# Kernel tuning notes

Hardware: AMD Instinct MI355X
Metric: run time of the kernel (lower is better)

## Reference

```python
import jax, jax.numpy as jnp
import numpy as np

DIM, QK, GS, DEPTH, VOCAB, ROT = 16, 128, 256, 8, 1024, 32
EPS = 1e-5


def scale_norm(x, g):
    # ScaleNorm: x / max(||x|| * dim^-0.5, eps) * g
    norm = jnp.linalg.norm(x, axis=-1, keepdims=True) * (DIM ** -0.5)
    return x / jnp.clip(norm, EPS) * g


def rotate_half(x):
    # interleaved pairs: (x0,x1,x2,x3,...) -> (-x1,x0,-x3,x2,...)
    xr = x.reshape(x.shape[:-1] + (-1, 2))
    a, b = xr[..., 0], xr[..., 1]
    return jnp.stack((-b, a), axis=-1).reshape(x.shape)


def apply_rotary(x, cos, sin):
    # rotary applied to first ROT dims only
    xr, xp = x[..., :ROT], x[..., ROT:]
    return jnp.concatenate([xr * cos + rotate_half(xr) * sin, xp], axis=-1)


def flash_layer(x, p, cos, sin, keymask, n):
    b = x.shape[0]
    normed = scale_norm(x, p['norm_g'])
    # shift_tokens: first half of channels shifted forward by one position
    xs, xp = jnp.split(normed, 2, axis=-1)
    xs = jnp.pad(xs, ((0, 0), (1, 0), (0, 0)))[:, :-1]
    normed = jnp.concatenate([xs, xp], axis=-1)
    hid = jax.nn.silu(normed @ p['Wh'] + p['bh'])  # [b,n,64]
    v, gate = jnp.split(hid, 2, axis=-1)           # each [b,n,32]
    qk = jax.nn.silu(normed @ p['Wqk'] + p['bqk'])  # [b,n,128]
    offs = qk[..., None, :] * p['gamma'] + p['beta']  # [b,n,4,128]
    quad_q, lin_q, quad_k, lin_k = [apply_rotary(offs[..., i, :], cos, sin) for i in range(4)]
    pad = (-n) % GS
    grp = lambda t: jnp.pad(t, ((0, 0), (0, pad), (0, 0))).reshape(b, -1, GS, t.shape[-1])
    quad_q, quad_k, lin_q, lin_k, vg = map(grp, (quad_q, quad_k, lin_q, lin_k, v))
    # quadratic (local, within-group) attention with ReLU^2
    sim = jnp.einsum('bgid,bgjd->bgij', quad_q, quad_k) / GS
    attn = jnp.square(jax.nn.relu(sim)) * keymask  # mask out padded keys
    quad_out = jnp.einsum('bgij,bgjd->bgid', attn, vg)
    # linear (global, across-group) attention, reduced over groups
    lin_kv = jnp.einsum('bgnd,bgne->bde', lin_k, vg) / n
    lin_out = jnp.einsum('bgnd,bde->bgne', lin_q, lin_kv)
    out = (quad_out + lin_out).reshape(b, -1, v.shape[-1])[:, :n]
    out = gate * out
    return out @ p['Wo'] + p['bo'] + x


def forward(kmer_data, token_emb, pos_scale, norm_g, Wh, bh, Wqk, bqk, gamma, beta, Wo, bo, final_g, Wl, bl, W1, b1, W2, b2):
    b, n = kmer_data.shape
    x = token_emb[kmer_data]  # [b,n,16]
    t = jnp.arange(n, dtype=jnp.float32)
    # ScaledSinuEmbedding
    inv = 1.0 / (10000.0 ** (jnp.arange(0, DIM, 2, dtype=jnp.float32) / DIM))
    sinu = t[:, None] * inv[None, :]
    pos = jnp.concatenate([jnp.sin(sinu), jnp.cos(sinu)], axis=-1) * pos_scale
    x = x + pos
    # rotary tables (dim 32, interleaved repeat)
    rinv = 1.0 / (10000.0 ** (jnp.arange(0, ROT, 2, dtype=jnp.float32) / ROT))
    rf = jnp.repeat(t[:, None] * rinv[None, :], 2, axis=-1)  # [n,32]
    cos, sin = jnp.cos(rf), jnp.sin(rf)
    # key mask for padded positions (996 -> 1024)
    pad = (-n) % GS
    keymask = jnp.pad(jnp.ones((n,), jnp.float32), (0, pad)).reshape(1, -1, 1, GS)
    for i in range(DEPTH):
        p = dict(norm_g=norm_g[i], Wh=Wh[i], bh=bh[i], Wqk=Wqk[i], bqk=bqk[i],
                 gamma=gamma[i], beta=beta[i], Wo=Wo[i], bo=bo[i])
        x = flash_layer(x, p, cos, sin, keymask, n)
    logits = scale_norm(x, final_g) @ Wl + bl  # [b,n,1024]
    h = jnp.max(logits, axis=-1)               # AdaptiveMaxPool1d(1) + Flatten -> [b,n]
    h = jax.nn.relu(h @ W1 + b1)
    return h @ W2 + b2                          # [b,1]


def setup_inputs() -> dict:
    key = jax.random.key(0)
    ks = jax.random.split(key, 12)
    r = lambda k, shape, s: jax.random.normal(k, shape, jnp.float32) * s
    return {
        'kmer_data': jax.random.randint(ks[0], (128, 996), 0, VOCAB),
        'token_emb': r(ks[1], (VOCAB, DIM), 1.0),
        'pos_scale': jnp.float32(1.0),
        'norm_g': jnp.ones((DEPTH,), jnp.float32),
        'Wh': r(ks[2], (DEPTH, DIM, 64), 0.1),
        'bh': jnp.zeros((DEPTH, 64), jnp.float32),
        'Wqk': r(ks[3], (DEPTH, DIM, QK), 0.1),
        'bqk': jnp.zeros((DEPTH, QK), jnp.float32),
        'gamma': 1.0 + r(ks[4], (DEPTH, 4, QK), 0.02),
        'beta': r(ks[5], (DEPTH, 4, QK), 0.02),
        'Wo': r(ks[6], (DEPTH, 32, DIM), 0.1),
        'bo': jnp.zeros((DEPTH, DIM), jnp.float32),
        'final_g': jnp.float32(1.0),
        'Wl': r(ks[7], (DIM, VOCAB), 0.1),
        'bl': jnp.zeros((VOCAB,), jnp.float32),
        'W1': r(ks[8], (996, 32), 0.05),
        'b1': jnp.zeros((32,), jnp.float32),
        'W2': r(ks[9], (32, 1), 0.1),
        'b2': jnp.zeros((1,), jnp.float32),
    }


def reference(kmer_data, token_emb, pos_scale, norm_g, Wh, bh, Wqk, bqk, gamma, beta, Wo, bo, final_g, Wl, bl, W1, b1, W2, b2):
    return forward(kmer_data, token_emb, pos_scale, norm_g, Wh, bh, Wqk, bqk,
                   gamma, beta, Wo, bo, final_g, Wl, bl, W1, b1, W2, b2)
```

## Files before the change

### kernel.cpp

```cpp
#include <hip/hip_runtime.h>

typedef short s16x8 __attribute__((ext_vector_type(8)));
typedef float f32x4 __attribute__((ext_vector_type(4)));

#define NB    128
#define NTOK  996
#define NPAD  1024
#define NGRP  4
#define GSZ   256
#define NLAY  8

__device__ __forceinline__ float bf2f(unsigned short u){
    unsigned int v = ((unsigned int)u) << 16;
    return __uint_as_float(v);
}
__device__ __forceinline__ unsigned short f2bf(float f){
    unsigned int x = __float_as_uint(f);
    unsigned int r = (x + 0x7fffu + ((x >> 16) & 1u)) >> 16;
    return (unsigned short)r;
}
__device__ __forceinline__ unsigned int packbf(float a, float b){
    return (unsigned int)f2bf(a) | ((unsigned int)f2bf(b) << 16);
}
__device__ __forceinline__ float silu(float v){
    return v / (1.0f + __expf(-v));
}

__device__ __forceinline__ s16x8 derive_core(const unsigned short* __restrict__ qrow, int d0,
        float4 g0, float4 g1, float4 b0, float4 b1,
        const float* __restrict__ rp, bool rot){
    uint4 u = *(const uint4*)(qrow + d0);
    float y0 = bf2f((unsigned short)(u.x & 0xffffu))*g0.x + b0.x;
    float y1 = bf2f((unsigned short)(u.x >> 16))    *g0.y + b0.y;
    float y2 = bf2f((unsigned short)(u.y & 0xffffu))*g0.z + b0.z;
    float y3 = bf2f((unsigned short)(u.y >> 16))    *g0.w + b0.w;
    float y4 = bf2f((unsigned short)(u.z & 0xffffu))*g1.x + b1.x;
    float y5 = bf2f((unsigned short)(u.z >> 16))    *g1.y + b1.y;
    float y6 = bf2f((unsigned short)(u.w & 0xffffu))*g1.z + b1.z;
    float y7 = bf2f((unsigned short)(u.w >> 16))    *g1.w + b1.w;
    if (rot){
        float4 c4 = *(const float4*)(rp);
        float4 s4 = *(const float4*)(rp + 16);
        float a;
        a = y0; y0 = a*c4.x - y1*s4.x; y1 = y1*c4.x + a*s4.x;
        a = y2; y2 = a*c4.y - y3*s4.y; y3 = y3*c4.y + a*s4.y;
        a = y4; y4 = a*c4.z - y5*s4.z; y5 = y5*c4.z + a*s4.z;
        a = y6; y6 = a*c4.w - y7*s4.w; y7 = y7*c4.w + a*s4.w;
    }
    union { unsigned int uu[4]; s16x8 s; } r;
    r.uu[0] = packbf(y0, y1);
    r.uu[1] = packbf(y2, y3);
    r.uu[2] = packbf(y4, y5);
    r.uu[3] = packbf(y6, y7);
    return r.s;
}

__global__ __launch_bounds__(256) void k_embed(const int* __restrict__ kmer,
                                               const float* __restrict__ emb,
                                               const float* __restrict__ ps,
                                               float* __restrict__ x,
                                               float* __restrict__ rope){
    int gid = blockIdx.x * 256 + threadIdx.x;
    if (gid < NPAD){
        float tf2 = (float)gid;
        #pragma unroll
        for (int i = 0; i < 16; i++){
            float inv = expf(((float)(2*i) / 32.0f) * -9.210340371976184f);
            float ang = tf2 * inv;
            rope[gid*32 + i]      = cosf(ang);
            rope[gid*32 + 16 + i] = sinf(ang);
        }
    }
    if (gid >= NB * NTOK) return;
    int b = gid / NTOK;
    int tt = gid - b * NTOK;
    int idx = kmer[gid];
    const float* er = emb + (size_t)idx * 16;
    float pscale = ps[0];
    float tf = (float)tt;
    float* xr = x + (size_t)gid * 16;
    #pragma unroll
    for (int i = 0; i < 8; i++){
        float inv = expf(((float)(2*i) / 16.0f) * -9.210340371976184f);
        float ang = tf * inv;
        xr[i]     = er[i]     + sinf(ang) * pscale;
        xr[8 + i] = er[8 + i] + cosf(ang) * pscale;
    }
}

__global__ __launch_bounds__(256, 2) void k_pre(const float* __restrict__ x,
                                             const float* __restrict__ Wh, const float* __restrict__ bh,
                                             const float* __restrict__ Wqk, const float* __restrict__ bqk,
                                             const float* __restrict__ norm_g,
                                             const float* __restrict__ gamma, const float* __restrict__ beta,
                                             const float* __restrict__ rope, int layer,
                                             unsigned short* __restrict__ qk,
                                             unsigned short* __restrict__ vT,
                                             unsigned short* __restrict__ gateb,
                                             float* __restrict__ linkvp){
    __shared__ __align__(16) unsigned short WcT[192 * 40];
    __shared__ unsigned int nrm[256][4];
    __shared__ __align__(16) unsigned char arena[23040];
    unsigned short* As = (unsigned short*)arena;
    unsigned short* LkT = (unsigned short*)arena;
    unsigned short* Vt  = (unsigned short*)(arena + 18432);
    int tid = threadIdx.x;
    int qt = blockIdx.x & 3, b = blockIdx.x >> 2;
    const float* Whl = Wh  + (size_t)layer * 1024;
    const float* Wql = Wqk + (size_t)layer * 2048;
    const float* gLin = gamma + (size_t)layer * 512 + 384;
    const float* bLin = beta  + (size_t)layer * 512 + 384;
    for (int i = tid; i < 1024; i += 256){ int d = i >> 6, c = i & 63;  WcT[c*40 + d] = f2bf(Whl[i]); }
    for (int i = tid; i < 2048; i += 256){ int d = i >> 7, c = i & 127; WcT[(64 + c)*40 + d] = f2bf(Wql[i]); }
    if (tid < 192){
        int i = tid;
        float bv = (i < 64) ? bh[layer*64 + i] : bqk[layer*128 + (i - 64)];
        WcT[i*40 + 16] = f2bf(bv);
        WcT[i*40 + 17] = 0;
        unsigned int* zz = (unsigned int*)(WcT + i*40 + 18);
        #pragma unroll
        for (int k = 0; k < 7; k++) zz[k] = 0u;
    }
    int tt = qt*256 + tid;
    int tsafe = tt < NTOK ? tt : (NTOK - 1);
    float g = norm_g[layer];
    unsigned int* dd = (unsigned int*)(As + tid * 40);
    {
        const float4* xr4 = (const float4*)(x + ((size_t)b*NTOK + tsafe) * 16);
        float cur[16];
        float s2 = 0.f;
        #pragma unroll
        for (int c = 0; c < 4; c++){
            float4 v4 = xr4[c];
            cur[4*c] = v4.x; cur[4*c+1] = v4.y; cur[4*c+2] = v4.z; cur[4*c+3] = v4.w;
        }
        #pragma unroll
        for (int d = 0; d < 16; d++) s2 += cur[d]*cur[d];
        float sc = g / fmaxf(sqrtf(s2) * 0.25f, 1e-5f);
        #pragma unroll
        for (int i = 0; i < 4; i++) nrm[tid][i] = packbf(cur[2*i]*sc, cur[2*i+1]*sc);
        #pragma unroll
        for (int i = 0; i < 4; i++) dd[4 + i] = packbf(cur[8 + 2*i]*sc, cur[9 + 2*i]*sc);
        dd[8] = 0x00003f80u;
        #pragma unroll
        for (int i = 9; i < 16; i++) dd[i] = 0u;
    }
    __syncthreads();
    if (tt == 0){
        #pragma unroll
        for (int i = 0; i < 4; i++) dd[i] = 0u;
    } else if (tid > 0){
        #pragma unroll
        for (int i = 0; i < 4; i++) dd[i] = nrm[tid - 1][i];
    } else {
        const float4* xp4 = (const float4*)(x + ((size_t)b*NTOK + tt - 1) * 16);
        float prv[16]; float p2 = 0.f;
        #pragma unroll
        for (int c = 0; c < 4; c++){
            float4 v4 = xp4[c];
            prv[4*c] = v4.x; prv[4*c+1] = v4.y; prv[4*c+2] = v4.z; prv[4*c+3] = v4.w;
        }
        #pragma unroll
        for (int d = 0; d < 16; d++) p2 += prv[d]*prv[d];
        float sp = g / fmaxf(sqrtf(p2) * 0.25f, 1e-5f);
        #pragma unroll
        for (int i = 0; i < 4; i++) dd[i] = packbf(prv[2*i]*sp, prv[2*i+1]*sp);
    }
    __syncthreads();
    int w = tid >> 6, lane = tid & 63, m16 = lane & 15, quad = lane >> 4;
    s16x8 wf[12];
    #pragma unroll
    for (int mi = 0; mi < 12; mi++)
        wf[mi] = *(const s16x8*)(WcT + (mi*16 + m16)*40 + quad*8);
    s16x8 bfr[4];
    #pragma unroll
    for (int nt = 0; nt < 4; nt++)
        bfr[nt] = *(const s16x8*)(As + ((w*64 + nt*16 + m16))*40 + quad*8);
    __syncthreads();
    f32x4 zacc = {0.f,0.f,0.f,0.f};
    f32x4 lacc[2][2] = {{{0,0,0,0},{0,0,0,0}},{{0,0,0,0},{0,0,0,0}}};
    #pragma unroll
    for (int nt = 0; nt < 4; nt++){
        int tloc = w*64 + nt*16 + m16;
        int ttk = qt*256 + tloc;
        bool tv = ttk < NTOK;
        int c = w*16 + m16;
        size_t rowq = ((size_t)b*NPAD + ttk);
        #pragma unroll
        for (int mi = 0; mi < 12; mi++){
            f32x4 r = __builtin_amdgcn_mfma_f32_16x16x32_bf16(wf[mi], bfr[nt], zacc, 0, 0, 0);
            float sv[4];
            #pragma unroll
            for (int reg = 0; reg < 4; reg++) sv[reg] = silu(r[reg]);
            int wc0 = mi*16 + quad*4;
            if (mi < 2){
                #pragma unroll
                for (int reg = 0; reg < 4; reg++){
                    unsigned short pv = tv ? f2bf(sv[reg]) : (unsigned short)0;
                    vT[((size_t)b*32 + wc0 + reg)*NPAD + ttk] = pv;
                    Vt[(wc0 + reg)*72 + c] = pv;
                }
            } else if (mi < 4){
                *(uint2*)(gateb + rowq*32 + (wc0 - 32)) = make_uint2(packbf(sv[0],sv[1]), packbf(sv[2],sv[3]));
            } else {
                int qd = wc0 - 64;
                *(uint2*)(qk + rowq*128 + qd) = make_uint2(packbf(sv[0],sv[1]), packbf(sv[2],sv[3]));
                float y0 = sv[0]*gLin[qd]   + bLin[qd];
                float y1 = sv[1]*gLin[qd+1] + bLin[qd+1];
                float y2 = sv[2]*gLin[qd+2] + bLin[qd+2];
                float y3 = sv[3]*gLin[qd+3] + bLin[qd+3];
                if (qd < 32){
                    const float* rp = rope + ttk*32 + (qd >> 1);
                    float c0 = rp[0], s0 = rp[16], c1 = rp[1], s1 = rp[17];
                    float a;
                    a = y0; y0 = a*c0 - y1*s0; y1 = y1*c0 + a*s0;
                    a = y2; y2 = a*c1 - y3*s1; y3 = y3*c1 + a*s1;
                }
                LkT[(qd+0)*72 + c] = f2bf(y0);
                LkT[(qd+1)*72 + c] = f2bf(y1);
                LkT[(qd+2)*72 + c] = f2bf(y2);
                LkT[(qd+3)*72 + c] = f2bf(y3);
            }
        }
        __syncthreads();
        #pragma unroll
        for (int ks2 = 0; ks2 < 2; ks2++){
            s16x8 a0 = *(const s16x8*)(LkT + ((2*w  )*16 + m16)*72 + ks2*32 + quad*8);
            s16x8 a1 = *(const s16x8*)(LkT + ((2*w+1)*16 + m16)*72 + ks2*32 + quad*8);
            s16x8 b0 = *(const s16x8*)(Vt + (m16)*72 + ks2*32 + quad*8);
            s16x8 b1 = *(const s16x8*)(Vt + (16 + m16)*72 + ks2*32 + quad*8);
            lacc[0][0] = __builtin_amdgcn_mfma_f32_16x16x32_bf16(a0, b0, lacc[0][0], 0,0,0);
            lacc[0][1] = __builtin_amdgcn_mfma_f32_16x16x32_bf16(a0, b1, lacc[0][1], 0,0,0);
            lacc[1][0] = __builtin_amdgcn_mfma_f32_16x16x32_bf16(a1, b0, lacc[1][0], 0,0,0);
            lacc[1][1] = __builtin_amdgcn_mfma_f32_16x16x32_bf16(a1, b1, lacc[1][1], 0,0,0);
        }
        __syncthreads();
    }
    const float invn = 1.0f / 996.0f;
    #pragma unroll
    for (int i = 0; i < 2; i++){
        #pragma unroll
        for (int j = 0; j < 2; j++){
            int e = j*16 + m16;
            #pragma unroll
            for (int reg = 0; reg < 4; reg++){
                int d = (2*w + i)*16 + quad*4 + reg;
                linkvp[(((size_t)qt*NB + b)*32 + e)*128 + d] = lacc[i][j][reg] * invn;
            }
        }
    }
}

#define KD_BYTES (64*136*2)
#define PW_BYTES (8*32*72*2)
__global__ __launch_bounds__(512, 2) void k_quad(const unsigned short* __restrict__ qk,
                                              const unsigned short* __restrict__ vT,
                                              const unsigned short* __restrict__ gateb,
                                              const float* __restrict__ linkvp,
                                              const float* __restrict__ rope,
                                              const float* __restrict__ gamma, const float* __restrict__ beta,
                                              int layer,
                                              const float* __restrict__ Wo, const float* __restrict__ bo,
                                              float* __restrict__ x){
    __shared__ __align__(16) unsigned char smem[KD_BYTES + PW_BYTES];
    __shared__ __align__(16) unsigned short LkBs[32 * 136];
    __shared__ float sWo[512];
    __shared__ float sbo[16];
    unsigned short* Kd = (unsigned short*)smem;
    unsigned short* Pw = (unsigned short*)(smem + KD_BYTES);
    int tid = threadIdx.x;
    int blk = blockIdx.x;
    int g = blk & 3, b = blk >> 2;
    int tg0 = g * GSZ;
    const float* gamL = gamma + (size_t)layer * 512;
    const float* betL = beta  + (size_t)layer * 512;
    sWo[tid] = Wo[layer*512 + tid];
    if (tid < 16) sbo[tid] = bo[layer*16 + tid];

    int w = tid >> 6, lane = tid & 63, m16 = lane & 15, quad = lane >> 4;

    int tqA = tg0 + w*32 + m16;
    int tqB = tqA + 16;
    const unsigned short* qrowA = qk + ((size_t)b*NPAD + tqA)*128;
    const unsigned short* qrowB = qk + ((size_t)b*NPAD + tqB)*128;
    const float* rpA = rope + tqA*32 + quad*4;
    const float* rpB = rope + tqB*32 + quad*4;
    s16x8 qf[2][4];
    #pragma unroll
    for (int ks = 0; ks < 4; ks++){
        int d0 = ks*32 + quad*8;
        float4 g0 = *(const float4*)(gamL + d0), g1 = *(const float4*)(gamL + d0 + 4);
        float4 b0 = *(const float4*)(betL + d0), b1 = *(const float4*)(betL + d0 + 4);
        bool rot = (ks == 0) && (quad < 4);
        qf[0][ks] = derive_core(qrowA, d0, g0,g1,b0,b1, rpA, rot);
        qf[1][ks] = derive_core(qrowB, d0, g0,g1,b0,b1, rpB, rot);
    }

    const float* gK = gamL + 256;
    const float* bK = betL + 256;
    f32x4 oacc[2][2] = {{{0,0,0,0},{0,0,0,0}},{{0,0,0,0},{0,0,0,0}}};
    unsigned short* myP = Pw + w*32*72;

    for (int ch = 0; ch < 4; ch++){
        __syncthreads();
        {
            int r = tid >> 3, seg = (tid & 7) * 16;
            int tk = tg0 + ch*64 + r;
            const unsigned short* krow = qk + ((size_t)b*NPAD + tk)*128 + seg;
            unsigned int* dst = (unsigned int*)(Kd + r*136 + seg);
            #pragma unroll
            for (int h = 0; h < 2; h++){
                uint4 u = ((const uint4*)krow)[h];
                unsigned int uu[4] = {u.x, u.y, u.z, u.w};
                float y[8];
                #pragma unroll
                for (int k = 0; k < 4; k++){
                    int d = h*8 + 2*k;
                    y[2*k]   = bf2f((unsigned short)(uu[k] & 0xffffu)) * gK[seg + d]     + bK[seg + d];
                    y[2*k+1] = bf2f((unsigned short)(uu[k] >> 16))     * gK[seg + d + 1] + bK[seg + d + 1];
                }
                if (seg < 32){
                    const float* rp = rope + tk*32 + (seg >> 1) + h*4;
                    #pragma unroll
                    for (int p = 0; p < 4; p++){
                        float c = rp[p], s = rp[16 + p];
                        float a = y[2*p], d = y[2*p+1];
                        y[2*p]   = a*c - d*s;
                        y[2*p+1] = d*c + a*s;
                    }
                }
                #pragma unroll
                for (int k = 0; k < 4; k++) dst[h*4 + k] = packbf(y[2*k], y[2*k+1]);
            }
        }
        __syncthreads();
        #pragma unroll
        for (int np = 0; np < 2; np++){
            f32x4 s00 = {0,0,0,0}, s01 = {0,0,0,0}, s10 = {0,0,0,0}, s11 = {0,0,0,0};
            #pragma unroll
            for (int ks = 0; ks < 4; ks++){
                s16x8 kf0 = *(const s16x8*)(Kd + ((np*2  )*16 + m16)*136 + ks*32 + quad*8);
                s16x8 kf1 = *(const s16x8*)(Kd + ((np*2+1)*16 + m16)*136 + ks*32 + quad*8);
                s00 = __builtin_amdgcn_mfma_f32_16x16x32_bf16(qf[0][ks], kf0, s00, 0,0,0);
                s01 = __builtin_amdgcn_mfma_f32_16x16x32_bf16(qf[0][ks], kf1, s01, 0,0,0);
                s10 = __builtin_amdgcn_mfma_f32_16x16x32_bf16(qf[1][ks], kf0, s10, 0,0,0);
                s11 = __builtin_amdgcn_mfma_f32_16x16x32_bf16(qf[1][ks], kf1, s11, 0,0,0);
            }
            #pragma unroll
            for (int j = 0; j < 2; j++){
                int kl = (np*2 + j)*16 + m16;
                bool kv = (tg0 + ch*64 + kl) < NTOK;
                #pragma unroll
                for (int reg = 0; reg < 4; reg++){
                    float a0 = fmaxf(j ? s01[reg] : s00[reg], 0.0f);
                    float a1 = fmaxf(j ? s11[reg] : s10[reg], 0.0f);
                    a0 = a0 * a0;
                    a1 = a1 * a1;
                    myP[(quad*4 + reg)*72 + kl]      = kv ? f2bf(a0) : (unsigned short)0;
                    myP[(16 + quad*4 + reg)*72 + kl] = kv ? f2bf(a1) : (unsigned short)0;
                }
            }
        }
        #pragma unroll
        for (int i = 0; i < 2; i++){
            #pragma unroll
            for (int ks = 0; ks < 2; ks++){
                s16x8 pa = *(const s16x8*)(myP + (i*16 + m16)*72 + ks*32 + quad*8);
                s16x8 vf0 = *(const s16x8*)(vT + ((size_t)b*32 + m16)*NPAD + tg0 + ch*64 + ks*32 + quad*8);
                s16x8 vf1 = *(const s16x8*)(vT + ((size_t)b*32 + 16 + m16)*NPAD + tg0 + ch*64 + ks*32 + quad*8);
                oacc[i][0] = __builtin_amdgcn_mfma_f32_16x16x32_bf16(pa, vf0, oacc[i][0], 0,0,0);
                oacc[i][1] = __builtin_amdgcn_mfma_f32_16x16x32_bf16(pa, vf1, oacc[i][1], 0,0,0);
            }
        }
    }
    const float qsc = 1.0f / 65536.0f;
    #pragma unroll
    for (int i = 0; i < 2; i++)
        #pragma unroll
        for (int j = 0; j < 2; j++)
            oacc[i][j] = oacc[i][j] * qsc;
    {
        int e = tid >> 4, dbase = (tid & 15) * 8;
        float s[8];
        #pragma unroll
        for (int k = 0; k < 8; k++) s[k] = 0.f;
        #pragma unroll
        for (int part = 0; part < 4; part++){
            const float* src = linkvp + (((size_t)part*NB + b)*32 + e)*128 + dbase;
            float4 u0 = *(const float4*)src;
            float4 u1 = *(const float4*)(src + 4);
            s[0]+=u0.x; s[1]+=u0.y; s[2]+=u0.z; s[3]+=u0.w;
            s[4]+=u1.x; s[5]+=u1.y; s[6]+=u1.z; s[7]+=u1.w;
        }
        unsigned int* dst = (unsigned int*)(LkBs + e*136 + dbase);
        #pragma unroll
        for (int k = 0; k < 4; k++) dst[k] = packbf(s[2*k], s[2*k+1]);
    }
    __syncthreads();
    {
        const float* gamQ = gamL + 128;
        const float* betQ = betL + 128;
        #pragma unroll
        for (int ks = 0; ks < 4; ks++){
            int d0 = ks*32 + quad*8;
            float4 g0 = *(const float4*)(gamQ + d0), g1 = *(const float4*)(gamQ + d0 + 4);
            float4 b0 = *(const float4*)(betQ + d0), b1 = *(const float4*)(betQ + d0 + 4);
            bool rot = (ks == 0) && (quad < 4);
            s16x8 lf0 = derive_core(qrowA, d0, g0,g1,b0,b1, rpA, rot);
            s16x8 lf1 = derive_core(qrowB, d0, g0,g1,b0,b1, rpB, rot);
            #pragma unroll
            for (int j = 0; j < 2; j++){
                s16x8 lb = *(const s16x8*)(LkBs + (j*16 + m16)*136 + ks*32 + quad*8);
                oacc[0][j] = __builtin_amdgcn_mfma_f32_16x16x32_bf16(lf0, lb, oacc[0][j], 0,0,0);
                oacc[1][j] = __builtin_amdgcn_mfma_f32_16x16x32_bf16(lf1, lb, oacc[1][j], 0,0,0);
            }
        }
    }
    float* Obw = (float*)smem + w*1056;
    #pragma unroll
    for (int i = 0; i < 2; i++)
        #pragma unroll
        for (int j = 0; j < 2; j++)
            #pragma unroll
            for (int reg = 0; reg < 4; reg++)
                Obw[(i*16 + quad*4 + reg)*33 + j*16 + m16] = oacc[i][j][reg];
    {
        int r = lane >> 1, dp = (lane & 1) * 8;
        int p = tg0 + w*32 + r;
        if (p < NTOK){
            const unsigned short* gr = gateb + ((size_t)b*NPAD + p)*32;
            float* xr = x + ((size_t)b * NTOK + p)*16 + dp;
            float4 x0 = *(const float4*)xr;
            float4 x1 = *(const float4*)(xr + 4);
            float a[8] = { sbo[dp]+x0.x, sbo[dp+1]+x0.y, sbo[dp+2]+x0.z, sbo[dp+3]+x0.w,
                           sbo[dp+4]+x1.x, sbo[dp+5]+x1.y, sbo[dp+6]+x1.z, sbo[dp+7]+x1.w };
            #pragma unroll
            for (int eh = 0; eh < 4; eh++){
                uint4 gu = *(const uint4*)(gr + eh*8);
                unsigned int gg[4] = {gu.x, gu.y, gu.z, gu.w};
                #pragma unroll
                for (int k = 0; k < 4; k++){
                    float gv0 = bf2f((unsigned short)(gg[k] & 0xffffu));
                    float gv1 = bf2f((unsigned short)(gg[k] >> 16));
                    int e = eh*8 + 2*k;
                    float ov0 = Obw[r*33 + e] * gv0;
                    float ov1 = Obw[r*33 + e + 1] * gv1;
                    const float* wr0 = &sWo[e*16 + dp];
                    const float* wr1 = &sWo[(e+1)*16 + dp];
                    #pragma unroll
                    for (int kk = 0; kk < 8; kk++) a[kk] += ov0 * wr0[kk] + ov1 * wr1[kk];
                }
            }
            *(float4*)xr = make_float4(a[0],a[1],a[2],a[3]);
            *(float4*)(xr+4) = make_float4(a[4],a[5],a[6],a[7]);
        }
    }
}

__global__ __launch_bounds__(256) void k_head(const float* __restrict__ x,
                                              const float* __restrict__ Wl, const float* __restrict__ bl,
                                              const float* __restrict__ fg, float* __restrict__ h){
    __shared__ __align__(16) unsigned short WlT[512 * 40];
    __shared__ __align__(16) unsigned short As[256 * 40];
    int tid = threadIdx.x;
    int gid0 = blockIdx.x * 256;
    {
        int t = gid0 + tid;
        const float4* xr4 = (const float4*)(x + (size_t)t * 16);
        float cur[16]; float s2 = 0.f;
        #pragma unroll
        for (int c = 0; c < 4; c++){
            float4 v4 = xr4[c];
            cur[4*c] = v4.x; cur[4*c+1] = v4.y; cur[4*c+2] = v4.z; cur[4*c+3] = v4.w;
        }
        #pragma unroll
        for (int d = 0; d < 16; d++) s2 += cur[d]*cur[d];
        float sc = fg[0] / fmaxf(sqrtf(s2) * 0.25f, 1e-5f);
        unsigned int* dd = (unsigned int*)(As + tid * 40);
        #pragma unroll
        for (int i = 0; i < 8; i++) dd[i] = packbf(cur[2*i]*sc, cur[2*i+1]*sc);
        dd[8] = 0x00003f80u;
        #pragma unroll
        for (int i = 9; i < 16; i++) dd[i] = 0u;
    }
    int w = tid >> 6, lane = tid & 63, m16 = lane & 15, quad = lane >> 4;
    f32x4 vm[4];
    #pragma unroll
    for (int i = 0; i < 4; i++) vm[i] = (f32x4){-3e38f,-3e38f,-3e38f,-3e38f};
    for (int half = 0; half < 2; half++){
        __syncthreads();
        for (int i = tid; i < 8192; i += 256){
            int d = i >> 9, c = i & 511;
            WlT[c*40 + d] = f2bf(Wl[(size_t)d*1024 + half*512 + c]);
        }
        for (int i = tid; i < 512; i += 256){
            WlT[i*40 + 16] = f2bf(bl[half*512 + i]);
            WlT[i*40 + 17] = 0;
            unsigned int* zz = (unsigned int*)(WlT + i*40 + 18);
            #pragma unroll
            for (int k = 0; k < 7; k++) zz[k] = 0u;
        }
        __syncthreads();
        s16x8 af[4];
        #pragma unroll
        for (int i = 0; i < 4; i++)
            af[i] = *(const s16x8*)(As + (w*64 + i*16 + m16)*40 + quad*8);
        f32x4 zacc = {0,0,0,0};
        for (int nt = 0; nt < 32; nt++){
            s16x8 bf = *(const s16x8*)(WlT + (nt*16 + m16)*40 + quad*8);
            #pragma unroll
            for (int i = 0; i < 4; i++){
                f32x4 r = __builtin_amdgcn_mfma_f32_16x16x32_bf16(af[i], bf, zacc, 0,0,0);
                #pragma unroll
                for (int reg = 0; reg < 4; reg++)
                    vm[i][reg] = fmaxf(vm[i][reg], r[reg]);
            }
        }
    }
    #pragma unroll
    for (int i = 0; i < 4; i++){
        #pragma unroll
        for (int off = 1; off < 16; off <<= 1){
            #pragma unroll
            for (int reg = 0; reg < 4; reg++)
                vm[i][reg] = fmaxf(vm[i][reg], __shfl_xor(vm[i][reg], off, 64));
        }
    }
    if (m16 == 0){
        #pragma unroll
        for (int i = 0; i < 4; i++){
            int t0 = gid0 + w*64 + i*16 + quad*4;
            #pragma unroll
            for (int reg = 0; reg < 4; reg++)
                h[t0 + reg] = vm[i][reg];
        }
    }
}

__global__ __launch_bounds__(256) void k_final(const float* __restrict__ h,
                                               const float* __restrict__ W1, const float* __restrict__ b1,
                                               const float* __restrict__ W2, const float* __restrict__ b2,
                                               float* __restrict__ out){
    int b = blockIdx.x;
    int tid = threadIdx.x;
    int j = tid & 31, part = tid >> 5;
    float acc = 0.f;
    for (int i = part; i < NTOK; i += 8)
        acc += h[(size_t)b*NTOK + i] * W1[(size_t)i*32 + j];
    __shared__ float red[8][33];
    red[part][j] = acc;
    __syncthreads();
    if (tid < 32){
        float s = b1[tid];
        #pragma unroll
        for (int p = 0; p < 8; p++) s += red[p][tid];
        s = fmaxf(s, 0.f);
        red[0][tid] = s * W2[tid];
    }
    __syncthreads();
    if (tid == 0){
        float s = b2[0];
        #pragma unroll
        for (int jj = 0; jj < 32; jj++) s += red[0][jj];
        out[b] = s;
    }
}

extern "C" void kernel_launch(void* const* d_in, const int* in_sizes, int n_in,
                              void* d_out, int out_size, void* d_ws, size_t ws_size,
                              hipStream_t stream){
    const int*   kmer  = (const int*)d_in[0];
    const float* emb   = (const float*)d_in[1];
    const float* ps    = (const float*)d_in[2];
    const float* ng    = (const float*)d_in[3];
    const float* Wh    = (const float*)d_in[4];
    const float* bh    = (const float*)d_in[5];
    const float* Wqk   = (const float*)d_in[6];
    const float* bqk   = (const float*)d_in[7];
    const float* gamma = (const float*)d_in[8];
    const float* beta  = (const float*)d_in[9];
    const float* Wo    = (const float*)d_in[10];
    const float* bo    = (const float*)d_in[11];
    const float* fg    = (const float*)d_in[12];
    const float* Wl    = (const float*)d_in[13];
    const float* bl    = (const float*)d_in[14];
    const float* W1    = (const float*)d_in[15];
    const float* b1    = (const float*)d_in[16];
    const float* W2    = (const float*)d_in[17];
    const float* b2    = (const float*)d_in[18];
    float* out = (float*)d_out;

    char* wsp = (char*)d_ws;
    float* x = (float*)wsp;                     wsp += (size_t)NB*NTOK*16*4;
    unsigned short* qk = (unsigned short*)wsp;  wsp += (size_t)NB*NPAD*128*2;
    unsigned short* vT = (unsigned short*)wsp;  wsp += (size_t)NB*32*NPAD*2;
    unsigned short* gateb = (unsigned short*)wsp; wsp += (size_t)NB*NPAD*32*2;
    float* linkvp = (float*)wsp;                wsp += (size_t)4*NB*32*128*4;
    float* rope = (float*)wsp;                  wsp += (size_t)NPAD*32*4;
    float* h = (float*)wsp;                     wsp += (size_t)NB*NTOK*4;

    k_embed<<<(NB*NTOK + 255)/256, 256, 0, stream>>>(kmer, emb, ps, x, rope);
    for (int layer = 0; layer < NLAY; layer++){
        k_pre<<<NB*4, 256, 0, stream>>>(x, Wh, bh, Wqk, bqk, ng, gamma, beta, rope, layer, qk, vT, gateb, linkvp);
        k_quad<<<NB*NGRP, 512, 0, stream>>>(qk, vT, gateb, linkvp, rope, gamma, beta, layer, Wo, bo, x);
    }
    k_head<<<NB*NTOK/256, 256, 0, stream>>>(x, Wl, bl, fg, h);
    k_final<<<NB, 256, 0, stream>>>(h, W1, b1, W2, b2, out);
}
```

Baseline: 833.4 us.

## Widen k_pre to 512 threads, stage outputs via LDS, prefetch K and V in k_quad

k_pre now runs 512 threads per block, with each wave handling 32 tokens instead of 64. Its weight fragments are reloaded from LDS per MFMA rather than held in registers. qk, gate, vT and linkvp writes are buffered and emitted as coalesced vector stores through LDS transposes, and the shifted-token neighbour write goes straight into LDS, which drops one barrier. k_quad register-prefetches the next K chunk and its rope values, loads the V fragments early, hoists the gate and residual loads ahead of the epilogue, and raises launch bounds to 4 waves per SIMD occupancy. Together these aim to hide global latency and improve store coalescing, at the cost of more register and LDS pressure.

```diff
diff --git a/kernel.cpp b/kernel.cpp
--- a/kernel.cpp
+++ b/kernel.cpp
@@ -88,7 +88,7 @@
     }
 }
 
-__global__ __launch_bounds__(256, 2) void k_pre(const float* __restrict__ x,
+__global__ __launch_bounds__(512, 4) void k_pre(const float* __restrict__ x,
                                              const float* __restrict__ Wh, const float* __restrict__ bh,
                                              const float* __restrict__ Wqk, const float* __restrict__ bqk,
                                              const float* __restrict__ norm_g,
@@ -98,20 +98,19 @@
                                              unsigned short* __restrict__ vT,
                                              unsigned short* __restrict__ gateb,
                                              float* __restrict__ linkvp){
-    __shared__ __align__(16) unsigned short WcT[192 * 40];
-    __shared__ unsigned int nrm[256][4];
-    __shared__ __align__(16) unsigned char arena[23040];
-    unsigned short* As = (unsigned short*)arena;
-    unsigned short* LkT = (unsigned short*)arena;
-    unsigned short* Vt  = (unsigned short*)(arena + 18432);
+    __shared__ __align__(16) unsigned char sm[58880];
+    unsigned short* WcT = (unsigned short*)sm;
+    unsigned short* As  = (unsigned short*)(sm + 15360);
+    unsigned short* LkT = (unsigned short*)(sm + 15360);
+    unsigned short* Vt  = (unsigned short*)(sm + 50176);
     int tid = threadIdx.x;
     int qt = blockIdx.x & 3, b = blockIdx.x >> 2;
     const float* Whl = Wh  + (size_t)layer * 1024;
     const float* Wql = Wqk + (size_t)layer * 2048;
     const float* gLin = gamma + (size_t)layer * 512 + 384;
     const float* bLin = beta  + (size_t)layer * 512 + 384;
-    for (int i = tid; i < 1024; i += 256){ int d = i >> 6, c = i & 63;  WcT[c*40 + d] = f2bf(Whl[i]); }
-    for (int i = tid; i < 2048; i += 256){ int d = i >> 7, c = i & 127; WcT[(64 + c)*40 + d] = f2bf(Wql[i]); }
+    for (int i = tid; i < 1024; i += 512){ int d = i >> 6, c2 = i & 63;  WcT[c2*40 + d] = f2bf(Whl[i]); }
+    for (int i = tid; i < 2048; i += 512){ int d = i >> 7, c2 = i & 127; WcT[(64 + c2)*40 + d] = f2bf(Wql[i]); }
     if (tid < 192){
         int i = tid;
         float bv = (i < 64) ? bh[layer*64 + i] : bqk[layer*128 + (i - 64)];
@@ -121,90 +120,94 @@
         #pragma unroll
         for (int k = 0; k < 7; k++) zz[k] = 0u;
     }
-    int tt = qt*256 + tid;
-    int tsafe = tt < NTOK ? tt : (NTOK - 1);
     float g = norm_g[layer];
-    unsigned int* dd = (unsigned int*)(As + tid * 40);
-    {
+    if (tid < 256){
+        int tt = qt*256 + tid;
+        int tsafe = tt < NTOK ? tt : (NTOK - 1);
+        unsigned int* dd = (unsigned int*)(As + tid * 40);
         const float4* xr4 = (const float4*)(x + ((size_t)b*NTOK + tsafe) * 16);
         float cur[16];
         float s2 = 0.f;
         #pragma unroll
-        for (int c = 0; c < 4; c++){
-            float4 v4 = xr4[c];
-            cur[4*c] = v4.x; cur[4*c+1] = v4.y; cur[4*c+2] = v4.z; cur[4*c+3] = v4.w;
+        for (int c2 = 0; c2 < 4; c2++){
+            float4 v4 = xr4[c2];
+            cur[4*c2] = v4.x; cur[4*c2+1] = v4.y; cur[4*c2+2] = v4.z; cur[4*c2+3] = v4.w;
         }
         #pragma unroll
         for (int d = 0; d < 16; d++) s2 += cur[d]*cur[d];
         float sc = g / fmaxf(sqrtf(s2) * 0.25f, 1e-5f);
         #pragma unroll
-        for (int i = 0; i < 4; i++) nrm[tid][i] = packbf(cur[2*i]*sc, cur[2*i+1]*sc);
-        #pragma unroll
         for (int i = 0; i < 4; i++) dd[4 + i] = packbf(cur[8 + 2*i]*sc, cur[9 + 2*i]*sc);
         dd[8] = 0x00003f80u;
         #pragma unroll
         for (int i = 9; i < 16; i++) dd[i] = 0u;
-    }
-    __syncthreads();
-    if (tt == 0){
-        #pragma unroll
-        for (int i = 0; i < 4; i++) dd[i] = 0u;
-    } else if (tid > 0){
-        #pragma unroll
-        for (int i = 0; i < 4; i++) dd[i] = nrm[tid - 1][i];
-    } else {
-        const float4* xp4 = (const float4*)(x + ((size_t)b*NTOK + tt - 1) * 16);
-        float prv[16]; float p2 = 0.f;
-        #pragma unroll
-        for (int c = 0; c < 4; c++){
-            float4 v4 = xp4[c];
-            prv[4*c] = v4.x; prv[4*c+1] = v4.y; prv[4*c+2] = v4.z; prv[4*c+3] = v4.w;
-        }
-        #pragma unroll
-        for (int d = 0; d < 16; d++) p2 += prv[d]*prv[d];
-        float sp = g / fmaxf(sqrtf(p2) * 0.25f, 1e-5f);
-        #pragma unroll
-        for (int i = 0; i < 4; i++) dd[i] = packbf(prv[2*i]*sp, prv[2*i+1]*sp);
+        if (tid < 255){
+            unsigned int* ddn = (unsigned int*)(As + (tid+1) * 40);
+            #pragma unroll
+            for (int i = 0; i < 4; i++) ddn[i] = packbf(cur[2*i]*sc, cur[2*i+1]*sc);
+        }
+        if (tid == 0){
+            if (tt == 0){
+                dd[0] = 0u; dd[1] = 0u; dd[2] = 0u; dd[3] = 0u;
+            } else {
+                const float4* xp4 = (const float4*)(x + ((size_t)b*NTOK + tt - 1) * 16);
+                float prv[16]; float p2 = 0.f;
+                #pragma unroll
+                for (int c2 = 0; c2 < 4; c2++){
+                    float4 v4 = xp4[c2];
+                    prv[4*c2] = v4.x; prv[4*c2+1] = v4.y; prv[4*c2+2] = v4.z; prv[4*c2+3] = v4.w;
+                }
+                #pragma unroll
+                for (int d = 0; d < 16; d++) p2 += prv[d]*prv[d];
+                float sp = g / fmaxf(sqrtf(p2) * 0.25f, 1e-5f);
+                #pragma unroll
+                for (int i = 0; i < 4; i++) dd[i] = packbf(prv[2*i]*sp, prv[2*i+1]*sp);
+            }
+        }
     }
     __syncthreads();
     int w = tid >> 6, lane = tid & 63, m16 = lane & 15, quad = lane >> 4;
-    s16x8 wf[12];
-    #pragma unroll
-    for (int mi = 0; mi < 12; mi++)
-        wf[mi] = *(const s16x8*)(WcT + (mi*16 + m16)*40 + quad*8);
-    s16x8 bfr[4];
-    #pragma unroll
-    for (int nt = 0; nt < 4; nt++)
-        bfr[nt] = *(const s16x8*)(As + ((w*64 + nt*16 + m16))*40 + quad*8);
+    s16x8 bfr[2];
+    #pragma unroll
+    for (int nt = 0; nt < 2; nt++)
+        bfr[nt] = *(const s16x8*)(As + (w*32 + nt*16 + m16)*40 + quad*8);
     __syncthreads();
     f32x4 zacc = {0.f,0.f,0.f,0.f};
-    f32x4 lacc[2][2] = {{{0,0,0,0},{0,0,0,0}},{{0,0,0,0},{0,0,0,0}}};
-    #pragma unroll
-    for (int nt = 0; nt < 4; nt++){
-        int tloc = w*64 + nt*16 + m16;
-        int ttk = qt*256 + tloc;
+    f32x4 lacc[2] = {{0,0,0,0},{0,0,0,0}};
+    unsigned int qku[2][8][2];
+    unsigned int gu_[2][2][2];
+    unsigned int vpk[2][2][2];
+    int c = w*16 + m16;
+    #pragma unroll
+    for (int nt = 0; nt < 2; nt++){
+        int ttk = qt*256 + w*32 + nt*16 + m16;
         bool tv = ttk < NTOK;
-        int c = w*16 + m16;
-        size_t rowq = ((size_t)b*NPAD + ttk);
         #pragma unroll
         for (int mi = 0; mi < 12; mi++){
-            f32x4 r = __builtin_amdgcn_mfma_f32_16x16x32_bf16(wf[mi], bfr[nt], zacc, 0, 0, 0);
+            s16x8 wfm = *(const s16x8*)(WcT + (mi*16 + m16)*40 + quad*8);
+            f32x4 r = __builtin_amdgcn_mfma_f32_16x16x32_bf16(wfm, bfr[nt], zacc, 0, 0, 0);
             float sv[4];
             #pragma unroll
             for (int reg = 0; reg < 4; reg++) sv[reg] = silu(r[reg]);
             int wc0 = mi*16 + quad*4;
             if (mi < 2){
-                #pragma unroll
-                for (int reg = 0; reg < 4; reg++){
-                    unsigned short pv = tv ? f2bf(sv[reg]) : (unsigned short)0;
-                    vT[((size_t)b*32 + wc0 + reg)*NPAD + ttk] = pv;
-                    Vt[(wc0 + reg)*72 + c] = pv;
-                }
+                unsigned short p0 = tv ? f2bf(sv[0]) : (unsigned short)0;
+                unsigned short p1 = tv ? f2bf(sv[1]) : (unsigned short)0;
+                unsigned short p2 = tv ? f2bf(sv[2]) : (unsigned short)0;
+                unsigned short p3 = tv ? f2bf(sv[3]) : (unsigned short)0;
+                Vt[(wc0+0)*136 + c] = p0;
+                Vt[(wc0+1)*136 + c] = p1;
+                Vt[(wc0+2)*136 + c] = p2;
+                Vt[(wc0+3)*136 + c] = p3;
+                vpk[nt][mi][0] = (unsigned int)p0 | ((unsigned int)p1 << 16);
+                vpk[nt][mi][1] = (unsigned int)p2 | ((unsigned int)p3 << 16);
             } else if (mi < 4){
-                *(uint2*)(gateb + rowq*32 + (wc0 - 32)) = make_uint2(packbf(sv[0],sv[1]), packbf(sv[2],sv[3]));
+                gu_[nt][mi-2][0] = packbf(sv[0], sv[1]);
+                gu_[nt][mi-2][1] = packbf(sv[2], sv[3]);
             } else {
                 int qd = wc0 - 64;
-                *(uint2*)(qk + rowq*128 + qd) = make_uint2(packbf(sv[0],sv[1]), packbf(sv[2],sv[3]));
+                qku[nt][mi-4][0] = packbf(sv[0], sv[1]);
+                qku[nt][mi-4][1] = packbf(sv[2], sv[3]);
                 float y0 = sv[0]*gLin[qd]   + bLin[qd];
                 float y1 = sv[1]*gLin[qd+1] + bLin[qd+1];
                 float y2 = sv[2]*gLin[qd+2] + bLin[qd+2];
@@ -216,44 +219,74 @@
                     a = y0; y0 = a*c0 - y1*s0; y1 = y1*c0 + a*s0;
                     a = y2; y2 = a*c1 - y3*s1; y3 = y3*c1 + a*s1;
                 }
-                LkT[(qd+0)*72 + c] = f2bf(y0);
-                LkT[(qd+1)*72 + c] = f2bf(y1);
-                LkT[(qd+2)*72 + c] = f2bf(y2);
-                LkT[(qd+3)*72 + c] = f2bf(y3);
+                LkT[(qd+0)*136 + c] = f2bf(y0);
+                LkT[(qd+1)*136 + c] = f2bf(y1);
+                LkT[(qd+2)*136 + c] = f2bf(y2);
+                LkT[(qd+3)*136 + c] = f2bf(y3);
             }
         }
         __syncthreads();
         #pragma unroll
-        for (int ks2 = 0; ks2 < 2; ks2++){
-            s16x8 a0 = *(const s16x8*)(LkT + ((2*w  )*16 + m16)*72 + ks2*32 + quad*8);
-            s16x8 a1 = *(const s16x8*)(LkT + ((2*w+1)*16 + m16)*72 + ks2*32 + quad*8);
-            s16x8 b0 = *(const s16x8*)(Vt + (m16)*72 + ks2*32 + quad*8);
-            s16x8 b1 = *(const s16x8*)(Vt + (16 + m16)*72 + ks2*32 + quad*8);
-            lacc[0][0] = __builtin_amdgcn_mfma_f32_16x16x32_bf16(a0, b0, lacc[0][0], 0,0,0);
-            lacc[0][1] = __builtin_amdgcn_mfma_f32_16x16x32_bf16(a0, b1, lacc[0][1], 0,0,0);
-            lacc[1][0] = __builtin_amdgcn_mfma_f32_16x16x32_bf16(a1, b0, lacc[1][0], 0,0,0);
-            lacc[1][1] = __builtin_amdgcn_mfma_f32_16x16x32_bf16(a1, b1, lacc[1][1], 0,0,0);
+        for (int ks2 = 0; ks2 < 4; ks2++){
+            s16x8 a  = *(const s16x8*)(LkT + (w*16 + m16)*136 + ks2*32 + quad*8);
+            s16x8 b0 = *(const s16x8*)(Vt + (m16)*136 + ks2*32 + quad*8);
+            s16x8 b1 = *(const s16x8*)(Vt + (16 + m16)*136 + ks2*32 + quad*8);
+            lacc[0] = __builtin_amdgcn_mfma_f32_16x16x32_bf16(a, b0, lacc[0], 0,0,0);
+            lacc[1] = __builtin_amdgcn_mfma_f32_16x16x32_bf16(a, b1, lacc[1], 0,0,0);
         }
         __syncthreads();
     }
-    const float invn = 1.0f / 996.0f;
-    #pragma unroll
-    for (int i = 0; i < 2; i++){
-        #pragma unroll
-        for (int j = 0; j < 2; j++){
-            int e = j*16 + m16;
-            #pragma unroll
-            for (int reg = 0; reg < 4; reg++){
-                int d = (2*w + i)*16 + quad*4 + reg;
-                linkvp[(((size_t)qt*NB + b)*32 + e)*128 + d] = lacc[i][j][reg] * invn;
-            }
+    #pragma unroll
+    for (int nt = 0; nt < 2; nt++){
+        size_t rowq = (size_t)b*NPAD + qt*256 + w*32 + nt*16 + m16;
+        #pragma unroll
+        for (int mi8 = 0; mi8 < 8; mi8++)
+            *(uint2*)(qk + rowq*128 + mi8*16 + quad*4) = make_uint2(qku[nt][mi8][0], qku[nt][mi8][1]);
+        *(uint2*)(gateb + rowq*32 + quad*4)      = make_uint2(gu_[nt][0][0], gu_[nt][0][1]);
+        *(uint2*)(gateb + rowq*32 + 16 + quad*4) = make_uint2(gu_[nt][1][0], gu_[nt][1][1]);
+    }
+    {
+        unsigned short* mv = (unsigned short*)sm + w*1280;
+        #pragma unroll
+        for (int nt = 0; nt < 2; nt++){
+            #pragma unroll
+            for (int mi = 0; mi < 2; mi++){
+                int e0 = mi*16 + quad*4;
+                mv[(e0+0)*40 + nt*16 + m16] = (unsigned short)(vpk[nt][mi][0] & 0xffffu);
+                mv[(e0+1)*40 + nt*16 + m16] = (unsigned short)(vpk[nt][mi][0] >> 16);
+                mv[(e0+2)*40 + nt*16 + m16] = (unsigned short)(vpk[nt][mi][1] & 0xffffu);
+                mv[(e0+3)*40 + nt*16 + m16] = (unsigned short)(vpk[nt][mi][1] >> 16);
+            }
+        }
+        #pragma unroll
+        for (int r2 = 0; r2 < 2; r2++){
+            int e = r2*16 + (lane >> 2);
+            int cc = (lane & 3) * 8;
+            s16x8 vv = *(const s16x8*)(mv + e*40 + cc);
+            *(s16x8*)(vT + ((size_t)b*32 + e)*NPAD + qt*256 + w*32 + cc) = vv;
+        }
+    }
+    {
+        float* ml = (float*)(sm + 20480) + w*512;
+        const float invn = 1.0f / 996.0f;
+        #pragma unroll
+        for (int j = 0; j < 2; j++)
+            #pragma unroll
+            for (int reg = 0; reg < 4; reg++)
+                ml[(j*16 + m16)*16 + quad*4 + reg] = lacc[j][reg] * invn;
+        #pragma unroll
+        for (int r2 = 0; r2 < 2; r2++){
+            int e = r2*16 + (lane >> 2);
+            int dc = (lane & 3) * 4;
+            float4 vv = *(const float4*)(ml + e*16 + dc);
+            *(float4*)(linkvp + (((size_t)qt*NB + b)*32 + e)*128 + w*16 + dc) = vv;
         }
     }
 }
 
 #define KD_BYTES (64*136*2)
 #define PW_BYTES (8*32*72*2)
-__global__ __launch_bounds__(512, 2) void k_quad(const unsigned short* __restrict__ qk,
+__global__ __launch_bounds__(512, 4) void k_quad(const unsigned short* __restrict__ qk,
                                               const unsigned short* __restrict__ vT,
                                               const unsigned short* __restrict__ gateb,
                                               const float* __restrict__ linkvp,
@@ -301,16 +334,34 @@
     f32x4 oacc[2][2] = {{{0,0,0,0},{0,0,0,0}},{{0,0,0,0},{0,0,0,0}}};
     unsigned short* myP = Pw + w*32*72;
 
+    int kr = tid >> 3, seg = (tid & 7) * 16;
+    uint4 pku0, pku1;
+    float4 prc0, prc1, prs0, prs1;
+    auto LOADK = [&](int ch){
+        int tk = tg0 + ch*64 + kr;
+        const unsigned short* krow = qk + ((size_t)b*NPAD + tk)*128 + seg;
+        pku0 = ((const uint4*)krow)[0];
+        pku1 = ((const uint4*)krow)[1];
+        const float* rpk = rope + (seg < 32 ? (tk*32 + (seg >> 1)) : 0);
+        prc0 = *(const float4*)(rpk);
+        prs0 = *(const float4*)(rpk + 16);
+        prc1 = *(const float4*)(rpk + 4);
+        prs1 = *(const float4*)(rpk + 20);
+    };
+    LOADK(0);
+
     for (int ch = 0; ch < 4; ch++){
-        __syncthreads();
+        s16x8 vf[2][2];
+        #pragma unroll
+        for (int ks2 = 0; ks2 < 2; ks2++){
+            vf[ks2][0] = *(const s16x8*)(vT + ((size_t)b*32 + m16)*NPAD + tg0 + ch*64 + ks2*32 + quad*8);
+            vf[ks2][1] = *(const s16x8*)(vT + ((size_t)b*32 + 16 + m16)*NPAD + tg0 + ch*64 + ks2*32 + quad*8);
+        }
+        uint4 kd0, kd1;
         {
-            int r = tid >> 3, seg = (tid & 7) * 16;
-            int tk = tg0 + ch*64 + r;
-            const unsigned short* krow = qk + ((size_t)b*NPAD + tk)*128 + seg;
-            unsigned int* dst = (unsigned int*)(Kd + r*136 + seg);
             #pragma unroll
             for (int h = 0; h < 2; h++){
-                uint4 u = ((const uint4*)krow)[h];
+                uint4 u = h ? pku1 : pku0;
                 unsigned int uu[4] = {u.x, u.y, u.z, u.w};
                 float y[8];
                 #pragma unroll
@@ -320,19 +371,27 @@
                     y[2*k+1] = bf2f((unsigned short)(uu[k] >> 16))     * gK[seg + d + 1] + bK[seg + d + 1];
                 }
                 if (seg < 32){
-                    const float* rp = rope + tk*32 + (seg >> 1) + h*4;
+                    float cc[4], ss[4];
+                    if (h){ cc[0]=prc1.x; cc[1]=prc1.y; cc[2]=prc1.z; cc[3]=prc1.w;
+                            ss[0]=prs1.x; ss[1]=prs1.y; ss[2]=prs1.z; ss[3]=prs1.w; }
+                    else  { cc[0]=prc0.x; cc[1]=prc0.y; cc[2]=prc0.z; cc[3]=prc0.w;
+                            ss[0]=prs0.x; ss[1]=prs0.y; ss[2]=prs0.z; ss[3]=prs0.w; }
                     #pragma unroll
-                    for (int p = 0; p < 4; p++){
-                        float c = rp[p], s = rp[16 + p];
-                        float a = y[2*p], d = y[2*p+1];
-                        y[2*p]   = a*c - d*s;
-                        y[2*p+1] = d*c + a*s;
+                    for (int p2 = 0; p2 < 4; p2++){
+                        float a = y[2*p2], d2 = y[2*p2+1];
+                        y[2*p2]   = a*cc[p2] - d2*ss[p2];
+                        y[2*p2+1] = d2*cc[p2] + a*ss[p2];
                     }
                 }
-                #pragma unroll
-                for (int k = 0; k < 4; k++) dst[h*4 + k] = packbf(y[2*k], y[2*k+1]);
-            }
-        }
+                uint4 kk = make_uint4(packbf(y[0],y[1]), packbf(y[2],y[3]),
+                                      packbf(y[4],y[5]), packbf(y[6],y[7]));
+                if (h) kd1 = kk; else kd0 = kk;
+            }
+        }
+        __syncthreads();
+        *(uint4*)(Kd + kr*136 + seg)     = kd0;
+        *(uint4*)(Kd + kr*136 + seg + 8) = kd1;
+        if (ch < 3) LOADK(ch + 1);
         __syncthreads();
         #pragma unroll
         for (int np = 0; np < 2; np++){
@@ -364,12 +423,10 @@
         #pragma unroll
         for (int i = 0; i < 2; i++){
             #pragma unroll
-            for (int ks = 0; ks < 2; ks++){
-                s16x8 pa = *(const s16x8*)(myP + (i*16 + m16)*72 + ks*32 + quad*8);
-                s16x8 vf0 = *(const s16x8*)(vT + ((size_t)b*32 + m16)*NPAD + tg0 + ch*64 + ks*32 + quad*8);
-                s16x8 vf1 = *(const s16x8*)(vT + ((size_t)b*32 + 16 + m16)*NPAD + tg0 + ch*64 + ks*32 + quad*8);
-                oacc[i][0] = __builtin_amdgcn_mfma_f32_16x16x32_bf16(pa, vf0, oacc[i][0], 0,0,0);
-                oacc[i][1] = __builtin_amdgcn_mfma_f32_16x16x32_bf16(pa, vf1, oacc[i][1], 0,0,0);
+            for (int ks2 = 0; ks2 < 2; ks2++){
+                s16x8 pa = *(const s16x8*)(myP + (i*16 + m16)*72 + ks2*32 + quad*8);
+                oacc[i][0] = __builtin_amdgcn_mfma_f32_16x16x32_bf16(pa, vf[ks2][0], oacc[i][0], 0,0,0);
+                oacc[i][1] = __builtin_amdgcn_mfma_f32_16x16x32_bf16(pa, vf[ks2][1], oacc[i][1], 0,0,0);
             }
         }
     }
@@ -397,6 +454,17 @@
         for (int k = 0; k < 4; k++) dst[k] = packbf(s[2*k], s[2*k+1]);
     }
     __syncthreads();
+    int pr = lane >> 1, dp2 = (lane & 1) * 8;
+    int p = tg0 + w*32 + pr;
+    bool pvld = p < NTOK;
+    int psafe = pvld ? p : (NTOK - 1);
+    const unsigned short* gr = gateb + ((size_t)b*NPAD + psafe)*32;
+    uint4 egu[4];
+    #pragma unroll
+    for (int eh = 0; eh < 4; eh++) egu[eh] = *(const uint4*)(gr + eh*8);
+    float* xr = x + ((size_t)b*NTOK + psafe)*16 + dp2;
+    float4 ex0 = *(const float4*)xr;
+    float4 ex1 = *(const float4*)(xr + 4);
     {
         const float* gamQ = gamL + 128;
         const float* betQ = betL + 128;
@@ -424,36 +492,27 @@
             #pragma unroll
             for (int reg = 0; reg < 4; reg++)
                 Obw[(i*16 + quad*4 + reg)*33 + j*16 + m16] = oacc[i][j][reg];
-    {
-        int r = lane >> 1, dp = (lane & 1) * 8;
-        int p = tg0 + w*32 + r;
-        if (p < NTOK){
-            const unsigned short* gr = gateb + ((size_t)b*NPAD + p)*32;
-            float* xr = x + ((size_t)b * NTOK + p)*16 + dp;
-            float4 x0 = *(const float4*)xr;
-            float4 x1 = *(const float4*)(xr + 4);
-            float a[8] = { sbo[dp]+x0.x, sbo[dp+1]+x0.y, sbo[dp+2]+x0.z, sbo[dp+3]+x0.w,
-                           sbo[dp+4]+x1.x, sbo[dp+5]+x1.y, sbo[dp+6]+x1.z, sbo[dp+7]+x1.w };
-            #pragma unroll
-            for (int eh = 0; eh < 4; eh++){
-                uint4 gu = *(const uint4*)(gr + eh*8);
-                unsigned int gg[4] = {gu.x, gu.y, gu.z, gu.w};
+    if (pvld){
+        float a[8] = { sbo[dp2]+ex0.x, sbo[dp2+1]+ex0.y, sbo[dp2+2]+ex0.z, sbo[dp2+3]+ex0.w,
+                       sbo[dp2+4]+ex1.x, sbo[dp2+5]+ex1.y, sbo[dp2+6]+ex1.z, sbo[dp2+7]+ex1.w };
+        #pragma unroll
+        for (int eh = 0; eh < 4; eh++){
+            unsigned int gg[4] = {egu[eh].x, egu[eh].y, egu[eh].z, egu[eh].w};
+            #pragma unroll
+            for (int k = 0; k < 4; k++){
+                float gv0 = bf2f((unsigned short)(gg[k] & 0xffffu));
+                float gv1 = bf2f((unsigned short)(gg[k] >> 16));
+                int e = eh*8 + 2*k;
+                float ov0 = Obw[pr*33 + e] * gv0;
+                float ov1 = Obw[pr*33 + e + 1] * gv1;
+                const float* wr0 = &sWo[e*16 + dp2];
+                const float* wr1 = &sWo[(e+1)*16 + dp2];
                 #pragma unroll
-                for (int k = 0; k < 4; k++){
-                    float gv0 = bf2f((unsigned short)(gg[k] & 0xffffu));
-                    float gv1 = bf2f((unsigned short)(gg[k] >> 16));
-                    int e = eh*8 + 2*k;
-                    float ov0 = Obw[r*33 + e] * gv0;
-                    float ov1 = Obw[r*33 + e + 1] * gv1;
-                    const float* wr0 = &sWo[e*16 + dp];
-                    const float* wr1 = &sWo[(e+1)*16 + dp];
-                    #pragma unroll
-                    for (int kk = 0; kk < 8; kk++) a[kk] += ov0 * wr0[kk] + ov1 * wr1[kk];
-                }
-            }
-            *(float4*)xr = make_float4(a[0],a[1],a[2],a[3]);
-            *(float4*)(xr+4) = make_float4(a[4],a[5],a[6],a[7]);
-        }
+                for (int kk = 0; kk < 8; kk++) a[kk] += ov0 * wr0[kk] + ov1 * wr1[kk];
+            }
+        }
+        *(float4*)xr = make_float4(a[0],a[1],a[2],a[3]);
+        *(float4*)(xr+4) = make_float4(a[4],a[5],a[6],a[7]);
     }
 }
 
@@ -601,7 +660,7 @@
 
     k_embed<<<(NB*NTOK + 255)/256, 256, 0, stream>>>(kmer, emb, ps, x, rope);
     for (int layer = 0; layer < NLAY; layer++){
-        k_pre<<<NB*4, 256, 0, stream>>>(x, Wh, bh, Wqk, bqk, ng, gamma, beta, rope, layer, qk, vT, gateb, linkvp);
+        k_pre<<<NB*4, 512, 0, stream>>>(x, Wh, bh, Wqk, bqk, ng, gamma, beta, rope, layer, qk, vT, gateb, linkvp);
         k_quad<<<NB*NGRP, 512, 0, stream>>>(qk, vT, gateb, linkvp, rope, gamma, beta, layer, Wo, bo, x);
     }
     k_head<<<NB*NTOK/256, 256, 0, stream>>>(x, Wl, bl, fg, h);
```

New measurement: 1.244 ms. 49.2% more time.
